# Kernel optimization log

Hardware: AMD Instinct MI355X
Metric: run time of the kernel (lower is better)

The kernel has to match this reference:

```python
import jax, jax.numpy as jnp
import numpy as np

NV, NC = 4096, 16384        # n_vars, n_clauses
VL, CL = 8, 8               # vlabel_dim (ground_dim), clabel_dim
VE, CE = 128, 128           # vemb_dim, cemb_dim
ITERS = 4                   # max_iters
LN_EPS = 1e-5


def setup_inputs() -> dict:
    key = jax.random.key(0)
    ks = jax.random.split(key, 10)
    return {
        "vlabels": jax.random.normal(ks[0], (NV, VL), jnp.float32),
        "clabels": jax.random.normal(ks[1], (NC, CL), jnp.float32),
        "cmat_pos": jax.random.uniform(ks[2], (NC, NV), jnp.float32),
        "cmat_neg": jax.random.uniform(ks[3], (NC, NV), jnp.float32),
        "W_V_pos": jax.random.normal(ks[4], (VL + VE, CE), jnp.float32),
        "W_V_neg": jax.random.normal(ks[5], (VL + VE, CE), jnp.float32),
        "B_V": jax.random.normal(ks[6], (CE,), jnp.float32),
        "W_C_pos": jax.random.normal(ks[7], (CL + CE, VE), jnp.float32),
        "W_C_neg": jax.random.normal(ks[8], (CL + CE, VE), jnp.float32),
        "B_C": jax.random.normal(ks[9], (VE,), jnp.float32),
        "ln_gamma": jnp.ones((VE,), jnp.float32),
        "ln_beta": jnp.zeros((VE,), jnp.float32),
    }


def _layernorm(x, gamma, beta):
    mu = jnp.mean(x, axis=-1, keepdims=True)
    var = jnp.var(x, axis=-1, keepdims=True)
    return (x - mu) * jax.lax.rsqrt(var + LN_EPS) * gamma + beta


def reference(vlabels, clabels, cmat_pos, cmat_neg,
              W_V_pos, W_V_neg, B_V, W_C_pos, W_C_neg, B_C,
              ln_gamma, ln_beta):
    n_vars = vlabels.shape[0]
    vmat_pos = cmat_pos.T  # [NV, NC]
    vmat_neg = cmat_neg.T
    vembs0 = jnp.zeros((n_vars, VE), vlabels.dtype)

    def step(vembs, _):
        vs = jnp.concatenate([vlabels, vembs], axis=1)          # [NV, VL+VE]
        pv = vs @ W_V_pos                                       # [NV, CE]
        nv = vs @ W_V_neg
        cembs = jax.nn.relu(cmat_pos @ pv + cmat_neg @ nv + B_V)  # [NC, CE]
        cs = jnp.concatenate([clabels, cembs], axis=1)          # [NC, CL+CE]
        pc = cs @ W_C_pos                                       # [NC, VE]
        nc = cs @ W_C_neg
        v = jax.nn.relu(vmat_pos @ pc + vmat_neg @ nc + B_C)    # [NV, VE]
        v = _layernorm(v, ln_gamma, ln_beta)
        return v, None

    vembs, _ = jax.lax.scan(step, vembs0, None, length=ITERS)
    return vembs
```

## Files before the change

### kernel.cpp

```cpp
#include <hip/hip_runtime.h>

#define NVV 4096
#define NCC 16384

typedef __attribute__((ext_vector_type(8))) short short8;
typedef __attribute__((ext_vector_type(4))) short short4v;
typedef __attribute__((ext_vector_type(4))) float f32x4;

__device__ __forceinline__ short f2bf(float f) {
  union { float f; unsigned u; } v; v.f = f;
  unsigned r = v.u + 0x7fffu + ((v.u >> 16) & 1u);
  return (short)(r >> 16);
}

template<typename AT>
__device__ __forceinline__ short8 load8v(const AT* p) {
  if constexpr (sizeof(AT) == 2) {
    return *(const short8*)p;
  } else {
    const f32x4* q = (const f32x4*)p;
    f32x4 a = q[0], b = q[1];
    short8 o;
#pragma unroll
    for (int j = 0; j < 4; ++j) { o[j] = f2bf(a[j]); o[j + 4] = f2bf(b[j]); }
    return o;
  }
}

__global__ __launch_bounds__(256) void k_conv(const float* __restrict__ src,
                                              short* __restrict__ dst, int n8) {
  int i = blockIdx.x * blockDim.x + threadIdx.x;
  const int stride = gridDim.x * blockDim.x;
  for (; i < n8; i += stride) {
    const f32x4* q = (const f32x4*)(src + (size_t)i * 8);
    f32x4 a = q[0], b = q[1];
    short8 o;
#pragma unroll
    for (int j = 0; j < 4; ++j) { o[j] = f2bf(a[j]); o[j + 4] = f2bf(b[j]); }
    *(short8*)(dst + (size_t)i * 8) = o;
  }
}

__global__ __launch_bounds__(256) void k_convT(const float* __restrict__ src,
                                               short* __restrict__ dstN,
                                               short* __restrict__ dstT,
                                               int R, int C) {
  __shared__ short t[32][36];
  const int r0 = blockIdx.y * 32, c0 = blockIdx.x * 32;
  const int tr = threadIdx.x >> 3, tc4 = (threadIdx.x & 7) << 2;
  const f32x4 v = *(const f32x4*)(src + (size_t)(r0 + tr) * C + c0 + tc4);
  short4v o;
#pragma unroll
  for (int j = 0; j < 4; ++j) { o[j] = f2bf(v[j]); t[tc4 + j][tr] = o[j]; }
  *(short4v*)(dstN + (size_t)(r0 + tr) * C + c0 + tc4) = o;
  __syncthreads();
  short4v ot;
#pragma unroll
  for (int j = 0; j < 4; ++j) ot[j] = t[tr][tc4 + j];
  *(short4v*)(dstT + (size_t)(c0 + tr) * R + r0 + tc4) = ot;
}

template<bool FIRST, int NROW>
__global__ __launch_bounds__(128) void k_mlp(
    const float* __restrict__ labels, const float* __restrict__ embs,
    const float* __restrict__ Wp, const float* __restrict__ Wn,
    short* __restrict__ Tp, short* __restrict__ Tn, int Nrows) {
  const int n = threadIdx.x;
  const int m0 = blockIdx.x * NROW;
  float ap[NROW] = {}, an[NROW] = {};
  const int JMAX = FIRST ? 8 : 136;
  for (int j = 0; j < JMAX; ++j) {
    const float wp = Wp[j * 128 + n], wn = Wn[j * 128 + n];
#pragma unroll
    for (int r = 0; r < NROW; ++r) {
      const float x = (j < 8) ? labels[(size_t)(m0 + r) * 8 + j]
                              : embs[(size_t)(m0 + r) * 128 + (j - 8)];
      ap[r] = fmaf(x, wp, ap[r]);
      an[r] = fmaf(x, wn, an[r]);
    }
  }
  short4v vp, vn;
#pragma unroll
  for (int r = 0; r < NROW; ++r) { vp[r] = f2bf(ap[r]); vn[r] = f2bf(an[r]); }
  *(short4v*)(Tp + (size_t)n * Nrows + m0) = vp;
  *(short4v*)(Tn + (size_t)n * Nrows + m0) = vn;
}

template<int EPI>
__global__ __launch_bounds__(256) void k_gemm_f(
    const short* __restrict__ Ap, const short* __restrict__ An,
    const short* __restrict__ Bp, const short* __restrict__ Bn,
    const float* __restrict__ bias, float* __restrict__ C,
    int M, int lda, int ldb, int Klen) {
  __shared__ __align__(16) short sA[4][2048];
  const int tid = threadIdx.x;
  const int w = tid >> 6, l = tid & 63, lr = l & 15, lh = l >> 4;
  const int m0 = blockIdx.x * 32, n0 = blockIdx.y * 64;
  const int Koff = (int)blockIdx.z * Klen;
  const int T = (Klen >> 6) << 1;
  f32x4 acc0 = {0.f, 0.f, 0.f, 0.f}, acc1 = {0.f, 0.f, 0.f, 0.f};

  const int sm = tid >> 3;
  const int skc = (tid & 7) ^ (sm & 7);
  const size_t aRowOff = (size_t)(m0 + sm) * lda + Koff + (skc << 3);
  const size_t bRowOff = (size_t)(n0 + (w << 4) + lr) * ldb + Koff + (lh << 3);

  auto stageA = [&](int t, int buf) {
    const short* A = (t & 1) ? An : Ap;
    const short* g = A + aRowOff + ((t >> 1) << 6);
    __builtin_amdgcn_global_load_lds(
        (const __attribute__((address_space(1))) void*)g,
        (__attribute__((address_space(3))) void*)(&sA[buf][w << 9]),
        16, 0, 0);
  };
  auto loadB = [&](int t, short8& b0, short8& b1) {
    const short* B = (t & 1) ? Bn : Bp;
    const short* g = B + bRowOff + ((t >> 1) << 6);
    b0 = *(const short8*)g;
    b1 = *(const short8*)(g + 32);
  };

  stageA(0, 0);
  short8 bC0, bC1, bN0, bN1;
  loadB(0, bC0, bC1);
  stageA(1, 1);

  for (int t = 0; t < T; ++t) {
    const int t1 = (t + 1 < T) ? t + 1 : t + 1 - T;
    const int t2 = (t + 2 < T) ? t + 2 : t + 2 - T;
    loadB(t1, bN0, bN1);
    stageA(t2, (t + 2) & 3);
    asm volatile("s_waitcnt vmcnt(6)" ::: "memory");
    __builtin_amdgcn_s_barrier();
    asm volatile("" ::: "memory");
    const int buf = t & 3;
    const int kc0 = lh, kc1 = 4 + lh;
    const int ma = lr, mb = 16 + lr;
    short8 a00 = *(const short8*)&sA[buf][(ma << 6) + ((kc0 ^ (ma & 7)) << 3)];
    short8 a01 = *(const short8*)&sA[buf][(mb << 6) + ((kc0 ^ (mb & 7)) << 3)];
    short8 a10 = *(const short8*)&sA[buf][(ma << 6) + ((kc1 ^ (ma & 7)) << 3)];
    short8 a11 = *(const short8*)&sA[buf][(mb << 6) + ((kc1 ^ (mb & 7)) << 3)];
    acc0 = __builtin_amdgcn_mfma_f32_16x16x32_bf16(a00, bC0, acc0, 0, 0, 0);
    acc1 = __builtin_amdgcn_mfma_f32_16x16x32_bf16(a01, bC0, acc1, 0, 0, 0);
    acc0 = __builtin_amdgcn_mfma_f32_16x16x32_bf16(a10, bC1, acc0, 0, 0, 0);
    acc1 = __builtin_amdgcn_mfma_f32_16x16x32_bf16(a11, bC1, acc1, 0, 0, 0);
    bC0 = bN0; bC1 = bN1;
  }

  const int cn = n0 + (w << 4) + lr;
#pragma unroll
  for (int mf = 0; mf < 2; ++mf) {
    f32x4 a = mf ? acc1 : acc0;
#pragma unroll
    for (int r = 0; r < 4; ++r) {
      const int m = m0 + (mf << 4) + (lh << 2) + r;
      if (EPI == 0) {
        C[(size_t)m * 128 + cn] = fmaxf(a[r] + bias[cn], 0.f);
      } else {
        C[((size_t)blockIdx.z * M + m) * 128 + cn] = a[r];
      }
    }
  }
}

template<typename AT, bool TRANSA, int EPI>
__global__ __launch_bounds__(256) void k_gemm(
    const AT* __restrict__ Ap, const AT* __restrict__ An,
    const short* __restrict__ Bp, const short* __restrict__ Bn,
    const float* __restrict__ bias, float* __restrict__ C,
    int M, int lda, int ldb, int Klen) {
  __shared__ __align__(16) short sA[2][32 * 64];
  __shared__ __align__(16) short sB[2][64 * 64];
  const int tid = threadIdx.x;
  const int w = tid >> 6, l = tid & 63, lr = l & 15, lh = l >> 4;
  const int m0 = blockIdx.x * 32, n0 = blockIdx.y * 64;
  const int Koff = blockIdx.z * Klen;
  f32x4 acc0 = {0.f, 0.f, 0.f, 0.f}, acc1 = {0.f, 0.f, 0.f, 0.f};

  for (int step = 0; step < (Klen >> 6); ++step) {
    const int k0 = Koff + (step << 6);
    __syncthreads();
    if (!TRANSA) {
      const int m = tid >> 3, kc = tid & 7;
      const size_t ga = (size_t)(m0 + m) * lda + k0 + (kc << 3);
      const int ad = (m << 6) + ((kc ^ (m & 7)) << 3);
      *(short8*)&sA[0][ad] = load8v(Ap + ga);
      *(short8*)&sA[1][ad] = load8v(An + ga);
    } else {
      const int r = tid >> 2, c8 = (tid & 3) << 3;
      const size_t ga = (size_t)(k0 + r) * lda + m0 + c8;
      short8 vp = load8v(Ap + ga), vn = load8v(An + ga);
#pragma unroll
      for (int j = 0; j < 8; ++j) {
        const int m = c8 + j;
        const int ad = (m << 6) + ((((r >> 3)) ^ (m & 7)) << 3) + (r & 7);
        sA[0][ad] = vp[j];
        sA[1][ad] = vn[j];
      }
    }
#pragma unroll
    for (int i = 0; i < 2; ++i) {
      const int c = (i << 8) + tid;
      const int n = c >> 3, kc = c & 7;
      const size_t gb = (size_t)(n0 + n) * ldb + k0 + (kc << 3);
      const int ad = (n << 6) + ((kc ^ (n & 7)) << 3);
      *(short8*)&sB[0][ad] = *(const short8*)(Bp + gb);
      *(short8*)&sB[1][ad] = *(const short8*)(Bn + gb);
    }
    __syncthreads();
#pragma unroll
    for (int kh = 0; kh < 2; ++kh) {
      const int kc = (kh << 2) + lh;
      const int bn_ = (w << 4) + lr;
      short8 bp = *(short8*)&sB[0][(bn_ << 6) + ((kc ^ (bn_ & 7)) << 3)];
      short8 bnv = *(short8*)&sB[1][(bn_ << 6) + ((kc ^ (bn_ & 7)) << 3)];
      short8 a0p = *(short8*)&sA[0][(lr << 6) + ((kc ^ (lr & 7)) << 3)];
      short8 a0n = *(short8*)&sA[1][(lr << 6) + ((kc ^ (lr & 7)) << 3)];
      const int m1 = 16 + lr;
      short8 a1p = *(short8*)&sA[0][(m1 << 6) + ((kc ^ (m1 & 7)) << 3)];
      short8 a1n = *(short8*)&sA[1][(m1 << 6) + ((kc ^ (m1 & 7)) << 3)];
      acc0 = __builtin_amdgcn_mfma_f32_16x16x32_bf16(a0p, bp, acc0, 0, 0, 0);
      acc0 = __builtin_amdgcn_mfma_f32_16x16x32_bf16(a0n, bnv, acc0, 0, 0, 0);
      acc1 = __builtin_amdgcn_mfma_f32_16x16x32_bf16(a1p, bp, acc1, 0, 0, 0);
      acc1 = __builtin_amdgcn_mfma_f32_16x16x32_bf16(a1n, bnv, acc1, 0, 0, 0);
    }
  }
  const int n = n0 + (w << 4) + lr;
#pragma unroll
  for (int mf = 0; mf < 2; ++mf) {
    f32x4 a = mf ? acc1 : acc0;
#pragma unroll
    for (int r = 0; r < 4; ++r) {
      const int m = m0 + (mf << 4) + (lh << 2) + r;
      float c = a[r];
      if (EPI == 0) {
        c += bias[n];
        c = fmaxf(c, 0.f);
        C[(size_t)m * 128 + n] = c;
      } else {
        C[((size_t)blockIdx.z * M + m) * 128 + n] = c;
      }
    }
  }
}

__global__ __launch_bounds__(256) void k_reduce_ln(
    const float* __restrict__ part, const float* __restrict__ bias,
    const float* __restrict__ gamma, const float* __restrict__ beta,
    float* __restrict__ out) {
  const int w = threadIdx.x >> 6, l = threadIdx.x & 63;
  const int m = blockIdx.x * 4 + w;
  const int n0 = l << 1;
  float x0 = bias[n0], x1 = bias[n0 + 1];
#pragma unroll
  for (int ks = 0; ks < 4; ++ks) {
    const size_t o = ((size_t)ks * NVV + m) * 128 + n0;
    x0 += part[o];
    x1 += part[o + 1];
  }
  x0 = fmaxf(x0, 0.f);
  x1 = fmaxf(x1, 0.f);
  float s = x0 + x1, q = x0 * x0 + x1 * x1;
#pragma unroll
  for (int off = 32; off; off >>= 1) {
    s += __shfl_xor(s, off);
    q += __shfl_xor(q, off);
  }
  const float mu = s * (1.f / 128.f);
  const float var = q * (1.f / 128.f) - mu * mu;
  const float inv = 1.f / sqrtf(var + 1e-5f);
  out[(size_t)m * 128 + n0]     = (x0 - mu) * inv * gamma[n0] + beta[n0];
  out[(size_t)m * 128 + n0 + 1] = (x1 - mu) * inv * gamma[n0 + 1] + beta[n0 + 1];
}

extern "C" void kernel_launch(void* const* d_in, const int* in_sizes, int n_in,
                              void* d_out, int out_size, void* d_ws, size_t ws_size,
                              hipStream_t stream) {
  const float* vlabels  = (const float*)d_in[0];
  const float* clabels  = (const float*)d_in[1];
  const float* cmat_pos = (const float*)d_in[2];
  const float* cmat_neg = (const float*)d_in[3];
  const float* Wvp = (const float*)d_in[4];
  const float* Wvn = (const float*)d_in[5];
  const float* Bv  = (const float*)d_in[6];
  const float* Wcp = (const float*)d_in[7];
  const float* Wcn = (const float*)d_in[8];
  const float* Bc  = (const float*)d_in[9];
  const float* gam = (const float*)d_in[10];
  const float* bet = (const float*)d_in[11];
  float* out = (float*)d_out;

  char* base = (char*)d_ws;
  size_t off = 0;
  auto carve = [&](size_t b) -> void* {
    void* p = base + off;
    off += (b + 255) & ~(size_t)255;
    return p;
  };
  short* pvT  = (short*)carve((size_t)128 * NVV * 2);
  short* nvT  = (short*)carve((size_t)128 * NVV * 2);
  short* pcT  = (short*)carve((size_t)128 * NCC * 2);
  short* ncT  = (short*)carve((size_t)128 * NCC * 2);
  float* cemb = (float*)carve((size_t)NCC * 128 * 4);
  float* part = (float*)carve((size_t)4 * NVV * 128 * 4);
  short* cmPb = (short*)carve((size_t)NCC * NVV * 2);
  short* cmNb = (short*)carve((size_t)NCC * NVV * 2);
  const size_t needN = off;
  short* cmTP = (short*)carve((size_t)NCC * NVV * 2);
  short* cmTN = (short*)carve((size_t)NCC * NVV * 2);
  const size_t needT = off;
  const bool big  = ws_size >= needN;
  const bool bigT = ws_size >= needT;

  if (bigT) {
    k_convT<<<dim3(NVV / 32, NCC / 32), 256, 0, stream>>>(cmat_pos, cmPb, cmTP, NCC, NVV);
    k_convT<<<dim3(NVV / 32, NCC / 32), 256, 0, stream>>>(cmat_neg, cmNb, cmTN, NCC, NVV);
  } else if (big) {
    k_conv<<<4096, 256, 0, stream>>>(cmat_pos, cmPb, NCC * NVV / 8);
    k_conv<<<4096, 256, 0, stream>>>(cmat_neg, cmNb, NCC * NVV / 8);
  }

  for (int it = 0; it < 4; ++it) {
    if (it == 0)
      k_mlp<true, 4><<<NVV / 4, 128, 0, stream>>>(vlabels, nullptr, Wvp, Wvn, pvT, nvT, NVV);
    else
      k_mlp<false, 4><<<NVV / 4, 128, 0, stream>>>(vlabels, out, Wvp, Wvn, pvT, nvT, NVV);

    if (big)
      k_gemm_f<0><<<dim3(NCC / 32, 2, 1), 256, 0, stream>>>(
          cmPb, cmNb, pvT, nvT, Bv, cemb, NCC, NVV, NVV, NVV);
    else
      k_gemm<float, false, 0><<<dim3(NCC / 32, 2, 1), 256, 0, stream>>>(
          cmat_pos, cmat_neg, pvT, nvT, Bv, cemb, NCC, NVV, NVV, NVV);

    k_mlp<false, 4><<<NCC / 4, 128, 0, stream>>>(clabels, cemb, Wcp, Wcn, pcT, ncT, NCC);

    if (bigT)
      k_gemm_f<1><<<dim3(NVV / 32, 2, 4), 256, 0, stream>>>(
          cmTP, cmTN, pcT, ncT, nullptr, part, NVV, NCC, NCC, NCC / 4);
    else if (big)
      k_gemm<short, true, 1><<<dim3(NVV / 32, 2, 4), 256, 0, stream>>>(
          cmPb, cmNb, pcT, ncT, nullptr, part, NVV, NVV, NCC, NVV);
    else
      k_gemm<float, true, 1><<<dim3(NVV / 32, 2, 4), 256, 0, stream>>>(
          cmat_pos, cmat_neg, pcT, ncT, nullptr, part, NVV, NVV, NCC, NVV);

    k_reduce_ln<<<NVV / 4, 256, 0, stream>>>(part, Bc, gam, bet, out);
  }
}
```

Measured before the change: 1.681 ms.

## Widen GEMM tile to full 128 columns with split-K and fuse bias-relu into MLP

Replaces the bf16 GEMM kernel with one where each block computes all 128 output columns and interleaves pos/neg A tiles in LDS, so each A tile is read from memory once instead of twice across column blocks. Both GEMMs now use split-K (2 for the clause side, 8 for the variable side), writing partials. The clause-side bias+ReLU and the partial sum are folded into the clause MLP kernel via a shared-memory stage. The MLP kernels handle 16 rows per block with wider stores. The trade-off is more partial-buffer traffic and more registers per thread.

```diff
diff --git a/kernel.cpp b/kernel.cpp
--- a/kernel.cpp
+++ b/kernel.cpp
@@ -60,106 +60,139 @@
   *(short4v*)(dstT + (size_t)(c0 + tr) * R + r0 + tc4) = ot;
 }
 
-template<bool FIRST, int NROW>
+template<int SRC, int NROW>
 __global__ __launch_bounds__(128) void k_mlp(
     const float* __restrict__ labels, const float* __restrict__ embs,
+    const float* __restrict__ bias,
     const float* __restrict__ Wp, const float* __restrict__ Wn,
     short* __restrict__ Tp, short* __restrict__ Tn, int Nrows) {
+  __shared__ float xs[NROW][130];
   const int n = threadIdx.x;
   const int m0 = blockIdx.x * NROW;
+  if (SRC == 2) {
+#pragma unroll
+    for (int r = 0; r < NROW; ++r) {
+      const size_t m = m0 + r;
+      xs[r][n] = fmaxf(embs[m * 128 + n] + embs[((size_t)NCC + m) * 128 + n] + bias[n], 0.f);
+    }
+    __syncthreads();
+  }
   float ap[NROW] = {}, an[NROW] = {};
-  const int JMAX = FIRST ? 8 : 136;
+  const int JMAX = (SRC == 0) ? 8 : 136;
   for (int j = 0; j < JMAX; ++j) {
     const float wp = Wp[j * 128 + n], wn = Wn[j * 128 + n];
 #pragma unroll
     for (int r = 0; r < NROW; ++r) {
-      const float x = (j < 8) ? labels[(size_t)(m0 + r) * 8 + j]
-                              : embs[(size_t)(m0 + r) * 128 + (j - 8)];
+      float x;
+      if (j < 8)            x = labels[(size_t)(m0 + r) * 8 + j];
+      else if (SRC == 2)    x = xs[r][j - 8];
+      else                  x = embs[(size_t)(m0 + r) * 128 + (j - 8)];
       ap[r] = fmaf(x, wp, ap[r]);
       an[r] = fmaf(x, wn, an[r]);
     }
   }
-  short4v vp, vn;
-#pragma unroll
-  for (int r = 0; r < NROW; ++r) { vp[r] = f2bf(ap[r]); vn[r] = f2bf(an[r]); }
-  *(short4v*)(Tp + (size_t)n * Nrows + m0) = vp;
-  *(short4v*)(Tn + (size_t)n * Nrows + m0) = vn;
-}
-
-template<int EPI>
-__global__ __launch_bounds__(256) void k_gemm_f(
+  short8 vp0, vn0, vp1, vn1;
+#pragma unroll
+  for (int r = 0; r < 8; ++r) {
+    vp0[r] = f2bf(ap[r]); vn0[r] = f2bf(an[r]);
+    vp1[r] = f2bf(ap[8 + r]); vn1[r] = f2bf(an[8 + r]);
+  }
+  *(short8*)(Tp + (size_t)n * Nrows + m0) = vp0;
+  *(short8*)(Tp + (size_t)n * Nrows + m0 + 8) = vp1;
+  *(short8*)(Tn + (size_t)n * Nrows + m0) = vn0;
+  *(short8*)(Tn + (size_t)n * Nrows + m0 + 8) = vn1;
+}
+
+__global__ __launch_bounds__(256, 4) void k_gemm3(
     const short* __restrict__ Ap, const short* __restrict__ An,
     const short* __restrict__ Bp, const short* __restrict__ Bn,
-    const float* __restrict__ bias, float* __restrict__ C,
-    int M, int lda, int ldb, int Klen) {
-  __shared__ __align__(16) short sA[4][2048];
+    float* __restrict__ C, int M, int lda, int ldb, int Klen) {
+  __shared__ __align__(16) short sA[2][4][2048];
   const int tid = threadIdx.x;
   const int w = tid >> 6, l = tid & 63, lr = l & 15, lh = l >> 4;
-  const int m0 = blockIdx.x * 32, n0 = blockIdx.y * 64;
+  const int m0 = blockIdx.x * 32;
   const int Koff = (int)blockIdx.z * Klen;
-  const int T = (Klen >> 6) << 1;
-  f32x4 acc0 = {0.f, 0.f, 0.f, 0.f}, acc1 = {0.f, 0.f, 0.f, 0.f};
+  const int T = Klen >> 6;
 
   const int sm = tid >> 3;
   const int skc = (tid & 7) ^ (sm & 7);
-  const size_t aRowOff = (size_t)(m0 + sm) * lda + Koff + (skc << 3);
-  const size_t bRowOff = (size_t)(n0 + (w << 4) + lr) * ldb + Koff + (lh << 3);
+  const short* gAp = Ap + (size_t)(m0 + sm) * lda + Koff + (skc << 3);
+  const short* gAn = An + (size_t)(m0 + sm) * lda + Koff + (skc << 3);
+  const size_t b0o = (size_t)((w << 4) + lr) * ldb + Koff + (lh << 3);
+  const size_t b1o = b0o + (size_t)64 * ldb;
+  const short* gBp0 = Bp + b0o; const short* gBp1 = Bp + b1o;
+  const short* gBn0 = Bn + b0o; const short* gBn1 = Bn + b1o;
+
+  f32x4 acc00 = {0,0,0,0}, acc01 = {0,0,0,0}, acc10 = {0,0,0,0}, acc11 = {0,0,0,0};
+  short8 bp00, bp01, bp10, bp11, bn00, bn01, bn10, bn11;
 
   auto stageA = [&](int t, int buf) {
-    const short* A = (t & 1) ? An : Ap;
-    const short* g = A + aRowOff + ((t >> 1) << 6);
+    const int ko = t << 6;
     __builtin_amdgcn_global_load_lds(
-        (const __attribute__((address_space(1))) void*)g,
-        (__attribute__((address_space(3))) void*)(&sA[buf][w << 9]),
-        16, 0, 0);
+        (const __attribute__((address_space(1))) void*)(gAp + ko),
+        (__attribute__((address_space(3))) void*)(&sA[0][buf][w << 9]), 16, 0, 0);
+    __builtin_amdgcn_global_load_lds(
+        (const __attribute__((address_space(1))) void*)(gAn + ko),
+        (__attribute__((address_space(3))) void*)(&sA[1][buf][w << 9]), 16, 0, 0);
   };
-  auto loadB = [&](int t, short8& b0, short8& b1) {
-    const short* B = (t & 1) ? Bn : Bp;
-    const short* g = B + bRowOff + ((t >> 1) << 6);
-    b0 = *(const short8*)g;
-    b1 = *(const short8*)(g + 32);
+  auto loadB = [&](int t) {
+    const int ko = t << 6;
+    bp00 = *(const short8*)(gBp0 + ko);      bp01 = *(const short8*)(gBp0 + ko + 32);
+    bp10 = *(const short8*)(gBp1 + ko);      bp11 = *(const short8*)(gBp1 + ko + 32);
+    bn00 = *(const short8*)(gBn0 + ko);      bn01 = *(const short8*)(gBn0 + ko + 32);
+    bn10 = *(const short8*)(gBn1 + ko);      bn11 = *(const short8*)(gBn1 + ko + 32);
   };
 
   stageA(0, 0);
-  short8 bC0, bC1, bN0, bN1;
-  loadB(0, bC0, bC1);
+  loadB(0);
   stageA(1, 1);
 
+  const int r0 = lr, r1 = 16 + lr;
   for (int t = 0; t < T; ++t) {
-    const int t1 = (t + 1 < T) ? t + 1 : t + 1 - T;
-    const int t2 = (t + 2 < T) ? t + 2 : t + 2 - T;
-    loadB(t1, bN0, bN1);
-    stageA(t2, (t + 2) & 3);
-    asm volatile("s_waitcnt vmcnt(6)" ::: "memory");
+    asm volatile("s_waitcnt vmcnt(10)" ::: "memory");
     __builtin_amdgcn_s_barrier();
     asm volatile("" ::: "memory");
-    const int buf = t & 3;
-    const int kc0 = lh, kc1 = 4 + lh;
-    const int ma = lr, mb = 16 + lr;
-    short8 a00 = *(const short8*)&sA[buf][(ma << 6) + ((kc0 ^ (ma & 7)) << 3)];
-    short8 a01 = *(const short8*)&sA[buf][(mb << 6) + ((kc0 ^ (mb & 7)) << 3)];
-    short8 a10 = *(const short8*)&sA[buf][(ma << 6) + ((kc1 ^ (ma & 7)) << 3)];
-    short8 a11 = *(const short8*)&sA[buf][(mb << 6) + ((kc1 ^ (mb & 7)) << 3)];
-    acc0 = __builtin_amdgcn_mfma_f32_16x16x32_bf16(a00, bC0, acc0, 0, 0, 0);
-    acc1 = __builtin_amdgcn_mfma_f32_16x16x32_bf16(a01, bC0, acc1, 0, 0, 0);
-    acc0 = __builtin_amdgcn_mfma_f32_16x16x32_bf16(a10, bC1, acc0, 0, 0, 0);
-    acc1 = __builtin_amdgcn_mfma_f32_16x16x32_bf16(a11, bC1, acc1, 0, 0, 0);
-    bC0 = bN0; bC1 = bN1;
-  }
-
-  const int cn = n0 + (w << 4) + lr;
-#pragma unroll
-  for (int mf = 0; mf < 2; ++mf) {
-    f32x4 a = mf ? acc1 : acc0;
-#pragma unroll
-    for (int r = 0; r < 4; ++r) {
-      const int m = m0 + (mf << 4) + (lh << 2) + r;
-      if (EPI == 0) {
-        C[(size_t)m * 128 + cn] = fmaxf(a[r] + bias[cn], 0.f);
-      } else {
-        C[((size_t)blockIdx.z * M + m) * 128 + cn] = a[r];
-      }
-    }
+    const short* bA0 = &sA[0][t & 3][0];
+    const short* bA1 = &sA[1][t & 3][0];
+    const int k0c = lh, k1c = 4 + lh;
+    short8 ap0k0 = *(const short8*)&bA0[(r0 << 6) + ((k0c ^ (r0 & 7)) << 3)];
+    short8 ap1k0 = *(const short8*)&bA0[(r1 << 6) + ((k0c ^ (r1 & 7)) << 3)];
+    short8 ap0k1 = *(const short8*)&bA0[(r0 << 6) + ((k1c ^ (r0 & 7)) << 3)];
+    short8 ap1k1 = *(const short8*)&bA0[(r1 << 6) + ((k1c ^ (r1 & 7)) << 3)];
+    short8 an0k0 = *(const short8*)&bA1[(r0 << 6) + ((k0c ^ (r0 & 7)) << 3)];
+    short8 an1k0 = *(const short8*)&bA1[(r1 << 6) + ((k0c ^ (r1 & 7)) << 3)];
+    short8 an0k1 = *(const short8*)&bA1[(r0 << 6) + ((k1c ^ (r0 & 7)) << 3)];
+    short8 an1k1 = *(const short8*)&bA1[(r1 << 6) + ((k1c ^ (r1 & 7)) << 3)];
+    acc00 = __builtin_amdgcn_mfma_f32_16x16x32_bf16(ap0k0, bp00, acc00, 0, 0, 0);
+    acc10 = __builtin_amdgcn_mfma_f32_16x16x32_bf16(ap1k0, bp00, acc10, 0, 0, 0);
+    acc01 = __builtin_amdgcn_mfma_f32_16x16x32_bf16(ap0k0, bp10, acc01, 0, 0, 0);
+    acc11 = __builtin_amdgcn_mfma_f32_16x16x32_bf16(ap1k0, bp10, acc11, 0, 0, 0);
+    acc00 = __builtin_amdgcn_mfma_f32_16x16x32_bf16(ap0k1, bp01, acc00, 0, 0, 0);
+    acc10 = __builtin_amdgcn_mfma_f32_16x16x32_bf16(ap1k1, bp01, acc10, 0, 0, 0);
+    acc01 = __builtin_amdgcn_mfma_f32_16x16x32_bf16(ap0k1, bp11, acc01, 0, 0, 0);
+    acc11 = __builtin_amdgcn_mfma_f32_16x16x32_bf16(ap1k1, bp11, acc11, 0, 0, 0);
+    acc00 = __builtin_amdgcn_mfma_f32_16x16x32_bf16(an0k0, bn00, acc00, 0, 0, 0);
+    acc10 = __builtin_amdgcn_mfma_f32_16x16x32_bf16(an1k0, bn00, acc10, 0, 0, 0);
+    acc01 = __builtin_amdgcn_mfma_f32_16x16x32_bf16(an0k0, bn10, acc01, 0, 0, 0);
+    acc11 = __builtin_amdgcn_mfma_f32_16x16x32_bf16(an1k0, bn10, acc11, 0, 0, 0);
+    acc00 = __builtin_amdgcn_mfma_f32_16x16x32_bf16(an0k1, bn01, acc00, 0, 0, 0);
+    acc10 = __builtin_amdgcn_mfma_f32_16x16x32_bf16(an1k1, bn01, acc10, 0, 0, 0);
+    acc01 = __builtin_amdgcn_mfma_f32_16x16x32_bf16(an0k1, bn11, acc01, 0, 0, 0);
+    acc11 = __builtin_amdgcn_mfma_f32_16x16x32_bf16(an1k1, bn11, acc11, 0, 0, 0);
+    const int t1 = (t + 1 < T) ? t + 1 : 0;
+    const int t2 = (t + 2 < T) ? t + 2 : t + 2 - T;
+    loadB(t1);
+    stageA(t2, (t + 2) & 3);
+  }
+
+  const int cn0 = (w << 4) + lr;
+  const size_t cb = ((size_t)blockIdx.z * M + m0 + (lh << 2)) * 128;
+#pragma unroll
+  for (int r = 0; r < 4; ++r) {
+    C[cb + (size_t)r * 128 + cn0]            = acc00[r];
+    C[cb + (size_t)r * 128 + cn0 + 64]       = acc01[r];
+    C[cb + (size_t)(16 + r) * 128 + cn0]      = acc10[r];
+    C[cb + (size_t)(16 + r) * 128 + cn0 + 64] = acc11[r];
   }
 }
 
@@ -244,6 +277,7 @@
   }
 }
 
+template<int KS>
 __global__ __launch_bounds__(256) void k_reduce_ln(
     const float* __restrict__ part, const float* __restrict__ bias,
     const float* __restrict__ gamma, const float* __restrict__ beta,
@@ -253,7 +287,7 @@
   const int n0 = l << 1;
   float x0 = bias[n0], x1 = bias[n0 + 1];
 #pragma unroll
-  for (int ks = 0; ks < 4; ++ks) {
+  for (int ks = 0; ks < KS; ++ks) {
     const size_t o = ((size_t)ks * NVV + m) * 128 + n0;
     x0 += part[o];
     x1 += part[o + 1];
@@ -301,14 +335,16 @@
   short* nvT  = (short*)carve((size_t)128 * NVV * 2);
   short* pcT  = (short*)carve((size_t)128 * NCC * 2);
   short* ncT  = (short*)carve((size_t)128 * NCC * 2);
+  float* part = (float*)carve((size_t)2 * NCC * 128 * 4);
   float* cemb = (float*)carve((size_t)NCC * 128 * 4);
-  float* part = (float*)carve((size_t)4 * NVV * 128 * 4);
+  const size_t off_small = off;
   short* cmPb = (short*)carve((size_t)NCC * NVV * 2);
   short* cmNb = (short*)carve((size_t)NCC * NVV * 2);
   const size_t needN = off;
   short* cmTP = (short*)carve((size_t)NCC * NVV * 2);
   short* cmTN = (short*)carve((size_t)NCC * NVV * 2);
   const size_t needT = off;
+  (void)off_small;
   const bool big  = ws_size >= needN;
   const bool bigT = ws_size >= needT;
 
@@ -322,29 +358,32 @@
 
   for (int it = 0; it < 4; ++it) {
     if (it == 0)
-      k_mlp<true, 4><<<NVV / 4, 128, 0, stream>>>(vlabels, nullptr, Wvp, Wvn, pvT, nvT, NVV);
+      k_mlp<0, 16><<<NVV / 16, 128, 0, stream>>>(vlabels, nullptr, nullptr, Wvp, Wvn, pvT, nvT, NVV);
     else
-      k_mlp<false, 4><<<NVV / 4, 128, 0, stream>>>(vlabels, out, Wvp, Wvn, pvT, nvT, NVV);
-
-    if (big)
-      k_gemm_f<0><<<dim3(NCC / 32, 2, 1), 256, 0, stream>>>(
-          cmPb, cmNb, pvT, nvT, Bv, cemb, NCC, NVV, NVV, NVV);
-    else
+      k_mlp<1, 16><<<NVV / 16, 128, 0, stream>>>(vlabels, out, nullptr, Wvp, Wvn, pvT, nvT, NVV);
+
+    if (big) {
+      k_gemm3<<<dim3(NCC / 32, 1, 2), 256, 0, stream>>>(
+          cmPb, cmNb, pvT, nvT, part, NCC, NVV, NVV, NVV / 2);
+      k_mlp<2, 16><<<NCC / 16, 128, 0, stream>>>(clabels, part, Bv, Wcp, Wcn, pcT, ncT, NCC);
+    } else {
       k_gemm<float, false, 0><<<dim3(NCC / 32, 2, 1), 256, 0, stream>>>(
           cmat_pos, cmat_neg, pvT, nvT, Bv, cemb, NCC, NVV, NVV, NVV);
-
-    k_mlp<false, 4><<<NCC / 4, 128, 0, stream>>>(clabels, cemb, Wcp, Wcn, pcT, ncT, NCC);
-
-    if (bigT)
-      k_gemm_f<1><<<dim3(NVV / 32, 2, 4), 256, 0, stream>>>(
-          cmTP, cmTN, pcT, ncT, nullptr, part, NVV, NCC, NCC, NCC / 4);
-    else if (big)
+      k_mlp<1, 16><<<NCC / 16, 128, 0, stream>>>(clabels, cemb, nullptr, Wcp, Wcn, pcT, ncT, NCC);
+    }
+
+    if (bigT) {
+      k_gemm3<<<dim3(NVV / 32, 1, 8), 256, 0, stream>>>(
+          cmTP, cmTN, pcT, ncT, part, NVV, NCC, NCC, NCC / 8);
+      k_reduce_ln<8><<<NVV / 4, 256, 0, stream>>>(part, Bc, gam, bet, out);
+    } else if (big) {
       k_gemm<short, true, 1><<<dim3(NVV / 32, 2, 4), 256, 0, stream>>>(
           cmPb, cmNb, pcT, ncT, nullptr, part, NVV, NVV, NCC, NVV);
-    else
+      k_reduce_ln<4><<<NVV / 4, 256, 0, stream>>>(part, Bc, gam, bet, out);
+    } else {
       k_gemm<float, true, 1><<<dim3(NVV / 32, 2, 4), 256, 0, stream>>>(
           cmat_pos, cmat_neg, pcT, ncT, nullptr, part, NVV, NVV, NCC, NVV);
-
-    k_reduce_ln<<<NVV / 4, 256, 0, stream>>>(part, Bc, gam, bet, out);
-  }
-}
+      k_reduce_ln<4><<<NVV / 4, 256, 0, stream>>>(part, Bc, gam, bet, out);
+    }
+  }
+}
```

After: 1.917 ms. +14.0%, slower.
